# Performance work log

Hardware: AMD Instinct MI355X
Metric: run time of the kernel (lower is better)

## Reference

```python
import jax, jax.numpy as jnp
import numpy as np

B, S, H = 2, 4096, 1024  # batch, seq_len, hidden_size (= all_head_size)


def setup_inputs() -> dict:
    key = jax.random.key(0)
    ks = jax.random.split(key, 7)
    sc = 1.0 / np.sqrt(H)
    return {
        "hidden_states": jax.random.normal(ks[0], (B, S, H), dtype=jnp.float32),
        "Wq": jax.random.normal(ks[1], (H, H), dtype=jnp.float32) * sc,
        "bq": jnp.zeros((H,), dtype=jnp.float32),
        "Wk": jax.random.normal(ks[2], (H, H), dtype=jnp.float32) * sc,
        "bk": jnp.zeros((H,), dtype=jnp.float32),
        "Wv": jax.random.normal(ks[3], (H, H), dtype=jnp.float32) * sc,
        "bv": jnp.zeros((H,), dtype=jnp.float32),
    }


def reference(hidden_states, Wq, bq, Wk, bk, Wv, bv):
    # QKV projections (weights stored as [in, out] = W.T of torch Linear)
    q = hidden_states @ Wq + bq  # [B,S,H]
    k = hidden_states @ Wk + bk
    v = hidden_states @ Wv + bv
    # Raw attention: no head split, no 1/sqrt(d) scaling (faithful to source)
    scores = jnp.einsum("bqh,bkh->bqk", q, k)  # [B,S,S]
    probs = jax.nn.softmax(scores, axis=-1)
    context = jnp.einsum("bqk,bkh->bqh", probs, v)  # [B,S,H]
    return context
```

## Files before the change

kernel.cpp:

```cpp
#include <hip/hip_runtime.h>
#include <stdint.h>

typedef __attribute__((ext_vector_type(8))) short short8;
typedef __attribute__((ext_vector_type(8))) _Float16 half8;
typedef __attribute__((ext_vector_type(4))) float f32x4;

__device__ __forceinline__ unsigned short f2h(float x) {
  _Float16 h = (_Float16)x;
  return __builtin_bit_cast(unsigned short, h);
}
__device__ __forceinline__ float h2f(unsigned short u) {
  return (float)__builtin_bit_cast(_Float16, u);
}

#define GLOAD16(gsrc, ldst)                                              \
  __builtin_amdgcn_global_load_lds(                                      \
      (const __attribute__((address_space(1))) void*)(gsrc),             \
      (__attribute__((address_space(3))) void*)(ldst), 16, 0, 0)

#define VM(N) asm volatile("s_waitcnt vmcnt(" #N ")" ::: "memory")
#define BARSYNC __builtin_amdgcn_s_barrier()

__global__ __launch_bounds__(256) void split_pair_f16_kernel(
    const float* __restrict__ in, unsigned short* __restrict__ h,
    unsigned short* __restrict__ l) {
  size_t i = (size_t)blockIdx.x * 256 + threadIdx.x;
  float4 a = ((const float4*)in)[2 * i];
  float4 b = ((const float4*)in)[2 * i + 1];
  ushort4 h0 = make_ushort4(f2h(a.x), f2h(a.y), f2h(a.z), f2h(a.w));
  ushort4 h1 = make_ushort4(f2h(b.x), f2h(b.y), f2h(b.z), f2h(b.w));
  ((ushort4*)h)[2 * i] = h0;
  ((ushort4*)h)[2 * i + 1] = h1;
  ((ushort4*)l)[2 * i] = make_ushort4(
      f2h(a.x - h2f(h0.x)), f2h(a.y - h2f(h0.y)),
      f2h(a.z - h2f(h0.z)), f2h(a.w - h2f(h0.w)));
  ((ushort4*)l)[2 * i + 1] = make_ushort4(
      f2h(b.x - h2f(h1.x)), f2h(b.y - h2f(h1.y)),
      f2h(b.z - h2f(h1.z)), f2h(b.w - h2f(h1.w)));
}

__global__ __launch_bounds__(256) void transpose_f16_kernel(
    const float* __restrict__ W, unsigned short* __restrict__ hT,
    int Kd, int Nd) {
  __shared__ float tile[32][33];
  int r = threadIdx.x >> 3;
  int c = (threadIdx.x & 7) * 4;
  int k0 = blockIdx.y * 32, n0 = blockIdx.x * 32;
  float4 v = *(const float4*)&W[(size_t)(k0 + r) * Nd + n0 + c];
  tile[r][c] = v.x; tile[r][c + 1] = v.y; tile[r][c + 2] = v.z; tile[r][c + 3] = v.w;
  __syncthreads();
  size_t o = (size_t)(n0 + r) * Kd + k0 + c;
  *(ushort4*)&hT[o] = make_ushort4(f2h(tile[c + 0][r]), f2h(tile[c + 1][r]),
                                   f2h(tile[c + 2][r]), f2h(tile[c + 3][r]));
}

__global__ __launch_bounds__(512, 2) void qkv_kernel(
    const unsigned short* __restrict__ Ah, const unsigned short* __restrict__ Al,
    const unsigned short* __restrict__ WT, const float* __restrict__ bq,
    const float* __restrict__ bk, const float* __restrict__ bv,
    unsigned short* __restrict__ qh, unsigned short* __restrict__ kh,
    unsigned short* __restrict__ vT) {
  __shared__ __align__(16) char smem[3 * 40 * 1024];
  constexpr int lda = 1024, ldb = 1024, K = 1024;
  const int t = threadIdx.x, wid = t >> 6, lane = t & 63;
  const int waveM = wid >> 2, waveN = wid & 3;
  const int lr0 = lane & 15, lk0 = (lane >> 4) * 8;
  const int m0 = blockIdx.y * 256, n0 = blockIdx.x * 128;

  const unsigned short* slot_src[5];
#pragma unroll
  for (int s = 0; s < 5; ++s) {
    int si = 5 * wid + s;
    const unsigned short* p;
    if (si < 16)      p = Ah + (size_t)(m0 + si * 16 + lr0) * lda + lk0;
    else if (si < 32) p = Al + (size_t)(m0 + (si - 16) * 16 + lr0) * lda + lk0;
    else              p = WT + (size_t)(n0 + (si - 32) * 16 + lr0) * ldb + lk0;
    slot_src[s] = p;
  }

  const int NTILES = K >> 5;
  f32x4 acc[8][2] = {};

#pragma unroll
  for (int tt = 0; tt < 2; ++tt)
#pragma unroll
    for (int s = 0; s < 5; ++s)
      GLOAD16(slot_src[s] + (size_t)tt * 32,
              smem + tt * 40960 + (5 * wid + s) * 1024);
  VM(5);
  BARSYNC;
  __builtin_amdgcn_sched_barrier(0);

  for (int tile = 0; tile < NTILES; ++tile) {
    const int cur = tile % 3, nxt = (tile + 2) % 3;
    const bool do_stage = (tile + 2) < NTILES;
    const char* cb = smem + cur * 40960;
    char* nb = smem + nxt * 40960;
    half8 bf[2];
#pragma unroll
    for (int p = 0; p < 4; ++p) {
      half8 ahf[2], alf[2];
#pragma unroll
      for (int i = 0; i < 2; ++i) {
        int mg = waveM * 8 + 2 * p + i;
        ahf[i] = *(const half8*)(cb + mg * 1024 + lane * 16);
        alf[i] = *(const half8*)(cb + (16 + mg) * 1024 + lane * 16);
      }
      if (p == 0) {
#pragma unroll
        for (int j = 0; j < 2; ++j) {
          int ng = waveN * 2 + j;
          bf[j] = *(const half8*)(cb + (32 + ng) * 1024 + lane * 16);
        }
      }
      if (do_stage) {
        if (p == 0) {
          GLOAD16(slot_src[0] + (size_t)(tile + 2) * 32, nb + (5 * wid + 0) * 1024);
          GLOAD16(slot_src[1] + (size_t)(tile + 2) * 32, nb + (5 * wid + 1) * 1024);
        } else {
          const int slot = p + 1;
          GLOAD16(slot_src[slot] + (size_t)(tile + 2) * 32,
                  nb + (5 * wid + slot) * 1024);
        }
      }
      __builtin_amdgcn_s_setprio(1);
#pragma unroll
      for (int i = 0; i < 2; ++i)
#pragma unroll
        for (int j = 0; j < 2; ++j) {
          f32x4 c = acc[2 * p + i][j];
          c = __builtin_amdgcn_mfma_f32_16x16x32_f16(ahf[i], bf[j], c, 0, 0, 0);
          c = __builtin_amdgcn_mfma_f32_16x16x32_f16(alf[i], bf[j], c, 0, 0, 0);
          acc[2 * p + i][j] = c;
        }
      __builtin_amdgcn_s_setprio(0);
      if (p < 3) __builtin_amdgcn_s_barrier();
    }
    if (tile + 1 < NTILES) {
      if (do_stage) VM(5); else VM(0);
      BARSYNC;
      __builtin_amdgcn_sched_barrier(0);
    }
  }

  const int or0 = (lane >> 4) * 4;
  const int slab = n0 >> 10;
#pragma unroll
  for (int mm = 0; mm < 8; ++mm)
#pragma unroll
    for (int j = 0; j < 2; ++j)
#pragma unroll
      for (int r = 0; r < 4; ++r) {
        int row = m0 + waveM * 128 + mm * 16 + or0 + r;
        int col = (n0 & 1023) + waveN * 32 + j * 16 + lr0;
        float x = acc[mm][j][r];
        if (slab == 0) {
          qh[(size_t)row * 1024 + col] = f2h(x + bq[col]);
        } else if (slab == 1) {
          kh[(size_t)row * 1024 + col] = f2h(x + bk[col]);
        } else {
          vT[(size_t)col * 8192 + row] = f2h(x + bv[col]);
        }
      }
}

__global__ __launch_bounds__(512, 2) void g1q_kernel(
    const unsigned short* __restrict__ Abase, size_t Astr, int lda,
    const unsigned short* __restrict__ Bbase, size_t Bstr, int ldb,
    float* __restrict__ outF, size_t Ostr, int ldo, int K) {
  __shared__ __align__(16) char smem[3 * 32 * 1024];
  const int t = threadIdx.x, wid = t >> 6, lane = t & 63;
  const int waveM = wid >> 2, waveN = wid & 3;
  const int lr0 = lane & 15, lk0 = (lane >> 4) * 8;
  const int m0 = blockIdx.y * 256, n0 = blockIdx.x * 256;
  const unsigned short* A = Abase + (size_t)blockIdx.z * Astr;
  const unsigned short* B = Bbase + (size_t)blockIdx.z * Bstr;
  float* out = outF + (size_t)blockIdx.z * Ostr;

  const unsigned short* slot_src[4];
#pragma unroll
  for (int s = 0; s < 4; ++s) {
    int si = 4 * wid + s;
    const unsigned short* p;
    if (si < 16) p = A + (size_t)(m0 + si * 16 + lr0) * lda + lk0;
    else         p = B + (size_t)(n0 + (si - 16) * 16 + lr0) * ldb + lk0;
    slot_src[s] = p;
  }

  const int NTILES = K >> 5;
  f32x4 acc[8][4] = {};

#pragma unroll
  for (int tt = 0; tt < 2; ++tt)
#pragma unroll
    for (int s = 0; s < 4; ++s)
      GLOAD16(slot_src[s] + (size_t)tt * 32,
              smem + tt * 32768 + (4 * wid + s) * 1024);
  VM(4);
  BARSYNC;
  __builtin_amdgcn_sched_barrier(0);

  for (int tile = 0; tile < NTILES; ++tile) {
    const int cur = tile % 3, nxt = (tile + 2) % 3;
    const bool do_stage = (tile + 2) < NTILES;
    const char* cb = smem + cur * 32768;
    char* nb = smem + nxt * 32768;
    half8 bf[4];
#pragma unroll
    for (int p = 0; p < 4; ++p) {
      half8 af[2];
#pragma unroll
      for (int i = 0; i < 2; ++i) {
        int mg = waveM * 8 + 2 * p + i;
        af[i] = *(const half8*)(cb + mg * 1024 + lane * 16);
      }
      if (p == 0) {
#pragma unroll
        for (int j = 0; j < 4; ++j) {
          int ng = waveN * 4 + j;
          bf[j] = *(const half8*)(cb + 16384 + ng * 1024 + lane * 16);
        }
      }
      if (do_stage)
        GLOAD16(slot_src[p] + (size_t)(tile + 2) * 32,
                nb + (4 * wid + p) * 1024);
      __builtin_amdgcn_s_setprio(1);
#pragma unroll
      for (int i = 0; i < 2; ++i)
#pragma unroll
        for (int j = 0; j < 4; ++j)
          acc[2 * p + i][j] = __builtin_amdgcn_mfma_f32_16x16x32_f16(
              af[i], bf[j], acc[2 * p + i][j], 0, 0, 0);
      __builtin_amdgcn_s_setprio(0);
      if (p < 3) __builtin_amdgcn_s_barrier();
    }
    if (tile + 1 < NTILES) {
      if (do_stage) VM(4); else VM(0);
      BARSYNC;
      __builtin_amdgcn_sched_barrier(0);
    }
  }

  const int or0 = (lane >> 4) * 4;
#pragma unroll
  for (int mm = 0; mm < 8; ++mm)
#pragma unroll
    for (int j = 0; j < 4; ++j)
#pragma unroll
      for (int r = 0; r < 4; ++r)
        out[(size_t)(m0 + waveM * 128 + mm * 16 + or0 + r) * ldo +
            (n0 + waveN * 64 + j * 16 + lr0)] = acc[mm][j][r];
}

__global__ __launch_bounds__(512, 2) void g1_kernel(
    const unsigned short* __restrict__ Abase, size_t Astr, int lda,
    const unsigned short* __restrict__ Bbase, size_t Bstr, int ldb,
    float* __restrict__ outF, size_t Ostr, int ldo, int K) {
  __shared__ __align__(16) char smem[3 * 48 * 1024];
  const int t = threadIdx.x, wid = t >> 6, lane = t & 63;
  const int waveM = wid >> 2, waveN = wid & 3;
  const int lr0 = lane & 15, lk0 = (lane >> 4) * 8;
  const int m0 = blockIdx.y * 256, n0 = blockIdx.x * 128;
  const unsigned short* A = Abase + (size_t)blockIdx.z * Astr;
  const unsigned short* B = Bbase + (size_t)blockIdx.z * Bstr;
  float* out = outF + (size_t)blockIdx.z * Ostr;

  const unsigned short* slot_src[6];
#pragma unroll
  for (int s = 0; s < 6; ++s) {
    int si = 6 * wid + s;
    const unsigned short* p;
    if (si < 16)      p = A + (size_t)(m0 + si * 16 + lr0) * lda + lk0;
    else if (si < 32) p = A + (size_t)(m0 + (si - 16) * 16 + lr0) * lda + 32 + lk0;
    else if (si < 40) p = B + (size_t)(n0 + (si - 32) * 16 + lr0) * ldb + lk0;
    else              p = B + (size_t)(n0 + (si - 40) * 16 + lr0) * ldb + 32 + lk0;
    slot_src[s] = p;
  }

  const int NTILES = K >> 6;
  f32x4 acc[8][2] = {};

#pragma unroll
  for (int tt = 0; tt < 2; ++tt)
#pragma unroll
    for (int s = 0; s < 6; ++s)
      GLOAD16(slot_src[s] + (size_t)tt * 64,
              smem + tt * 49152 + (6 * wid + s) * 1024);
  VM(6);
  BARSYNC;
  __builtin_amdgcn_sched_barrier(0);

  for (int tile = 0; tile < NTILES; ++tile) {
    const int cur = tile % 3, nxt = (tile + 2) % 3;
    const bool do_stage = (tile + 2) < NTILES;
    const char* cb = smem + cur * 49152;
    char* nb = smem + nxt * 49152;
    half8 blo[2], bhi[2];
#pragma unroll
    for (int p = 0; p < 4; ++p) {
      half8 alo[2], ahi[2];
#pragma unroll
      for (int i = 0; i < 2; ++i) {
        int mg = waveM * 8 + 2 * p + i;
        alo[i] = *(const half8*)(cb + mg * 1024 + lane * 16);
        ahi[i] = *(const half8*)(cb + (16 + mg) * 1024 + lane * 16);
      }
      if (p == 0) {
#pragma unroll
        for (int j = 0; j < 2; ++j) {
          int ng = waveN * 2 + j;
          blo[j] = *(const half8*)(cb + (32 + ng) * 1024 + lane * 16);
          bhi[j] = *(const half8*)(cb + (40 + ng) * 1024 + lane * 16);
        }
      }
      if (do_stage && p < 3) {
#pragma unroll
        for (int s = 0; s < 2; ++s) {
          int slot = 2 * p + s;
          GLOAD16(slot_src[slot] + (size_t)(tile + 2) * 64,
                  nb + (6 * wid + slot) * 1024);
        }
      }
      __builtin_amdgcn_s_setprio(1);
#pragma unroll
      for (int i = 0; i < 2; ++i)
#pragma unroll
        for (int j = 0; j < 2; ++j) {
          f32x4 c = acc[2 * p + i][j];
          c = __builtin_amdgcn_mfma_f32_16x16x32_f16(alo[i], blo[j], c, 0, 0, 0);
          c = __builtin_amdgcn_mfma_f32_16x16x32_f16(ahi[i], bhi[j], c, 0, 0, 0);
          acc[2 * p + i][j] = c;
        }
      __builtin_amdgcn_s_setprio(0);
      if (p < 3) __builtin_amdgcn_s_barrier();
    }
    if (tile + 1 < NTILES) {
      if (do_stage) VM(6); else VM(0);
      BARSYNC;
      __builtin_amdgcn_sched_barrier(0);
    }
  }

  const int or0 = (lane >> 4) * 4;
#pragma unroll
  for (int mm = 0; mm < 8; ++mm)
#pragma unroll
    for (int j = 0; j < 2; ++j)
#pragma unroll
      for (int r = 0; r < 4; ++r)
        out[(size_t)(m0 + waveM * 128 + mm * 16 + or0 + r) * ldo +
            (n0 + waveN * 32 + j * 16 + lr0)] = acc[mm][j][r];
}

__global__ __launch_bounds__(256) void softmax_rows_kernel(
    const float* Sm, unsigned short* P, int ncol, int pld) {
  const int t = threadIdx.x;
  const float* srow = Sm + (size_t)blockIdx.x * ncol;
  float4 v[4];
  float m = -3.4e38f;
#pragma unroll
  for (int i = 0; i < 4; ++i) {
    v[i] = ((const float4*)srow)[t + 256 * i];
    m = fmaxf(m, fmaxf(fmaxf(v[i].x, v[i].y), fmaxf(v[i].z, v[i].w)));
  }
#pragma unroll
  for (int off = 32; off >= 1; off >>= 1) m = fmaxf(m, __shfl_down(m, off));
  __shared__ float redm[4];
  if ((t & 63) == 0) redm[t >> 6] = m;
  __syncthreads();
  m = fmaxf(fmaxf(redm[0], redm[1]), fmaxf(redm[2], redm[3]));
  float s = 0.f;
#pragma unroll
  for (int i = 0; i < 4; ++i) {
    v[i].x = __expf(v[i].x - m);
    v[i].y = __expf(v[i].y - m);
    v[i].z = __expf(v[i].z - m);
    v[i].w = __expf(v[i].w - m);
    s += v[i].x + v[i].y + v[i].z + v[i].w;
  }
#pragma unroll
  for (int off = 32; off >= 1; off >>= 1) s += __shfl_down(s, off);
  __shared__ float reds[4];
  if ((t & 63) == 0) reds[t >> 6] = s;
  __syncthreads();
  s = reds[0] + reds[1] + reds[2] + reds[3];
  float inv = 1.f / s;
  unsigned short* prow = P + (size_t)blockIdx.x * pld;
#pragma unroll
  for (int i = 0; i < 4; ++i) {
    ushort4 o = make_ushort4(f2h(v[i].x * inv), f2h(v[i].y * inv),
                             f2h(v[i].z * inv), f2h(v[i].w * inv));
    ((ushort4*)prow)[t + 256 * i] = o;
  }
}

extern "C" void kernel_launch(void* const* d_in, const int* in_sizes, int n_in,
                              void* d_out, int out_size, void* d_ws, size_t ws_size,
                              hipStream_t stream) {
  const float* hs = (const float*)d_in[0];
  const float* Wq = (const float*)d_in[1];
  const float* bq = (const float*)d_in[2];
  const float* Wk = (const float*)d_in[3];
  const float* bk = (const float*)d_in[4];
  const float* Wv = (const float*)d_in[5];
  const float* bv = (const float*)d_in[6];
  float* out = (float*)d_out;

  constexpr int Ss = 4096, Hh = 1024;
  constexpr int Mm = 8192;
  constexpr size_t TOK = (size_t)Ss * Hh;
  char* ws = (char*)d_ws;
  const size_t MB = 1024 * 1024;

  unsigned short* qh = (unsigned short*)(ws + 0 * MB);
  unsigned short* kh = (unsigned short*)(ws + 16 * MB);
  unsigned short* vT = (unsigned short*)(ws + 32 * MB);
  char* rb = ws + 48 * MB;
  unsigned short* hs_h = (unsigned short*)(rb + 0 * MB);
  unsigned short* hs_l = (unsigned short*)(rb + 16 * MB);
  unsigned short* WT = (unsigned short*)(rb + 32 * MB);
  float* Sf = (float*)rb;

  const bool big = ws_size >= (size_t)176 * MB;

  split_pair_f16_kernel<<<dim3(Mm * Hh / 2048), 256, 0, stream>>>(hs, hs_h, hs_l);
  transpose_f16_kernel<<<dim3(32, 32), 256, 0, stream>>>(Wq, WT, Hh, Hh);
  transpose_f16_kernel<<<dim3(32, 32), 256, 0, stream>>>(
      Wk, WT + (size_t)1024 * 1024, Hh, Hh);
  transpose_f16_kernel<<<dim3(32, 32), 256, 0, stream>>>(
      Wv, WT + (size_t)2048 * 1024, Hh, Hh);

  qkv_kernel<<<dim3(24, 32), 512, 0, stream>>>(
      hs_h, hs_l, WT, bq, bk, bv, qh, kh, vT);

  if (big) {
    g1q_kernel<<<dim3(16, 16, 2), 512, 0, stream>>>(
        qh, TOK, Hh, kh, TOK, Hh, Sf, (size_t)Ss * Ss, Ss, Hh);
    softmax_rows_kernel<<<dim3(2 * Ss), 256, 0, stream>>>(
        Sf, (unsigned short*)Sf, Ss, 2 * Ss);
    g1_kernel<<<dim3(8, 16, 2), 512, 0, stream>>>(
        (const unsigned short*)Sf, (size_t)Ss * 2 * Ss, 2 * Ss,
        vT, (size_t)Ss, Mm, out, TOK, Hh, Ss);
  } else {
    float* Sb = (float*)rb;
    unsigned short* Pb = (unsigned short*)(rb + 64 * MB);
    for (int b = 0; b < 2; ++b) {
      g1q_kernel<<<dim3(16, 16, 1), 512, 0, stream>>>(
          qh + b * TOK, 0, Hh, kh + b * TOK, 0, Hh, Sb, 0, Ss, Hh);
      softmax_rows_kernel<<<dim3(Ss), 256, 0, stream>>>(Sb, Pb, Ss, Ss);
      g1_kernel<<<dim3(8, 16, 1), 512, 0, stream>>>(
          Pb, 0, Ss, vT + (size_t)b * Ss, 0, Mm, out + b * TOK, 0, Hh, Ss);
    }
  }
}
```

Baseline: 433.6 us.

## Switch QKV GEMM to double buffering and drop intra-tile barriers

The QKV projection kernel moves from a three-stage LDS ring to two buffers. All next-tile global-to-LDS loads are now issued at the top of each tile, and the kernel waits for every outstanding load before the end-of-tile barrier. The launch bound now asks for four blocks per CU instead of two. In all three GEMM kernels the per-phase s_barrier calls inside the tile loop are removed and replaced by an lgkmcnt(0) wait before the final barrier. This cuts barrier overhead and LDS footprint to raise occupancy, at the cost of less prefetch depth and tighter register limits that may cause spills.

```diff
diff --git a/kernel.cpp b/kernel.cpp
--- a/kernel.cpp
+++ b/kernel.cpp
@@ -20,6 +20,11 @@
 
 #define VM(N) asm volatile("s_waitcnt vmcnt(" #N ")" ::: "memory")
 #define BARSYNC __builtin_amdgcn_s_barrier()
+#define LGKM0                                                \
+  do {                                                       \
+    asm volatile("s_waitcnt lgkmcnt(0)" ::: "memory");       \
+    __builtin_amdgcn_sched_barrier(0);                       \
+  } while (0)
 
 __global__ __launch_bounds__(256) void split_pair_f16_kernel(
     const float* __restrict__ in, unsigned short* __restrict__ h,
@@ -54,13 +59,13 @@
                                    f2h(tile[c + 2][r]), f2h(tile[c + 3][r]));
 }
 
-__global__ __launch_bounds__(512, 2) void qkv_kernel(
+__global__ __launch_bounds__(512, 4) void qkv_kernel(
     const unsigned short* __restrict__ Ah, const unsigned short* __restrict__ Al,
     const unsigned short* __restrict__ WT, const float* __restrict__ bq,
     const float* __restrict__ bk, const float* __restrict__ bv,
     unsigned short* __restrict__ qh, unsigned short* __restrict__ kh,
     unsigned short* __restrict__ vT) {
-  __shared__ __align__(16) char smem[3 * 40 * 1024];
+  __shared__ __align__(16) char smem[2 * 40 * 1024];
   constexpr int lda = 1024, ldb = 1024, K = 1024;
   const int t = threadIdx.x, wid = t >> 6, lane = t & 63;
   const int waveM = wid >> 2, waveN = wid & 3;
@@ -82,20 +87,21 @@
   f32x4 acc[8][2] = {};
 
 #pragma unroll
-  for (int tt = 0; tt < 2; ++tt)
-#pragma unroll
-    for (int s = 0; s < 5; ++s)
-      GLOAD16(slot_src[s] + (size_t)tt * 32,
-              smem + tt * 40960 + (5 * wid + s) * 1024);
-  VM(5);
+  for (int s = 0; s < 5; ++s)
+    GLOAD16(slot_src[s], smem + (5 * wid + s) * 1024);
+  VM(0);
   BARSYNC;
   __builtin_amdgcn_sched_barrier(0);
 
   for (int tile = 0; tile < NTILES; ++tile) {
-    const int cur = tile % 3, nxt = (tile + 2) % 3;
-    const bool do_stage = (tile + 2) < NTILES;
-    const char* cb = smem + cur * 40960;
-    char* nb = smem + nxt * 40960;
+    const char* cb = smem + (tile & 1) * 40960;
+    char* nb = smem + ((tile + 1) & 1) * 40960;
+    if (tile + 1 < NTILES) {
+#pragma unroll
+      for (int s = 0; s < 5; ++s)
+        GLOAD16(slot_src[s] + (size_t)(tile + 1) * 32,
+                nb + (5 * wid + s) * 1024);
+    }
     half8 bf[2];
 #pragma unroll
     for (int p = 0; p < 4; ++p) {
@@ -111,16 +117,6 @@
         for (int j = 0; j < 2; ++j) {
           int ng = waveN * 2 + j;
           bf[j] = *(const half8*)(cb + (32 + ng) * 1024 + lane * 16);
-        }
-      }
-      if (do_stage) {
-        if (p == 0) {
-          GLOAD16(slot_src[0] + (size_t)(tile + 2) * 32, nb + (5 * wid + 0) * 1024);
-          GLOAD16(slot_src[1] + (size_t)(tile + 2) * 32, nb + (5 * wid + 1) * 1024);
-        } else {
-          const int slot = p + 1;
-          GLOAD16(slot_src[slot] + (size_t)(tile + 2) * 32,
-                  nb + (5 * wid + slot) * 1024);
         }
       }
       __builtin_amdgcn_s_setprio(1);
@@ -134,10 +130,10 @@
           acc[2 * p + i][j] = c;
         }
       __builtin_amdgcn_s_setprio(0);
-      if (p < 3) __builtin_amdgcn_s_barrier();
     }
     if (tile + 1 < NTILES) {
-      if (do_stage) VM(5); else VM(0);
+      LGKM0;
+      VM(0);
       BARSYNC;
       __builtin_amdgcn_sched_barrier(0);
     }
@@ -232,9 +228,9 @@
           acc[2 * p + i][j] = __builtin_amdgcn_mfma_f32_16x16x32_f16(
               af[i], bf[j], acc[2 * p + i][j], 0, 0, 0);
       __builtin_amdgcn_s_setprio(0);
-      if (p < 3) __builtin_amdgcn_s_barrier();
     }
     if (tile + 1 < NTILES) {
+      LGKM0;
       if (do_stage) VM(4); else VM(0);
       BARSYNC;
       __builtin_amdgcn_sched_barrier(0);
@@ -332,9 +328,9 @@
           acc[2 * p + i][j] = c;
         }
       __builtin_amdgcn_s_setprio(0);
-      if (p < 3) __builtin_amdgcn_s_barrier();
     }
     if (tile + 1 < NTILES) {
+      LGKM0;
       if (do_stage) VM(6); else VM(0);
       BARSYNC;
       __builtin_amdgcn_sched_barrier(0);
```

Result: faster. 403.1 us (-7.0%).
